# Kernel optimization log

Measured on AMD Instinct MI355X. Metric: run time of the kernel, lower is better.

The kernel has to match this reference:

```python
import jax, jax.numpy as jnp
import numpy as np

HID = 128  # hardcoded in the original module (hyperparameters['hidden_sizes'])
BETA1, BETA2, ADAM_EPS = 0.9, 0.999, 1e-8  # torch.optim.Adam defaults


def _xavier(k, shape):
    lim = np.sqrt(6.0 / (shape[0] + shape[1]))
    return jax.random.uniform(k, shape, jnp.float32, -lim, lim)


def setup_inputs() -> dict:
    key = jax.random.key(0)
    k0, k1, k2 = jax.random.split(key, 3)
    input_size, output_size = 65536, 4096
    return {
        "x": jax.random.uniform(k0, (input_size,), jnp.float32),
        "W1": _xavier(k1, (input_size, HID)),
        "W2": _xavier(k2, (HID, output_size)),
        "b_in": jnp.zeros((input_size,), jnp.float32),
        "b_h": jnp.zeros((HID,), jnp.float32),
        "b_out": jnp.zeros((output_size,), jnp.float32),
        "hidden0": jnp.zeros((HID,), jnp.float32),
        "output0": jnp.zeros((output_size,), jnp.float32),
        "n_iterations": 256,
        "epsilon": 0.01,
    }


def _drho(s):
    # gradient mask of rho = clamp(s, 0, 1), matching torch clamp backward
    return ((s >= 0.0) & (s <= 1.0)).astype(s.dtype)


def reference(x, W1, W2, b_in, b_h, b_out, hidden0, output0, n_iterations, epsilon):
    r_x = jnp.clip(x, 0.0, 1.0)
    xW1 = r_x @ W1  # [HID], constant across iterations (input is clamped/fixed)

    def adam(p, g, m, v, t1):
        m = BETA1 * m + (1.0 - BETA1) * g
        v = BETA2 * v + (1.0 - BETA2) * g * g
        mhat = m / (1.0 - jnp.power(BETA1, t1))
        vhat = v / (1.0 - jnp.power(BETA2, t1))
        return p - epsilon * mhat / (jnp.sqrt(vhat) + ADAM_EPS), m, v

    def step(carry, t):
        h, o, mh, vh, mo, vo = carry
        r_h = jnp.clip(h, 0.0, 1.0)
        r_o = jnp.clip(o, 0.0, 1.0)
        # analytic dE/dh, dE/do of the quadratic Hopfield energy
        g_h = _drho(h) * (r_h - b_h - xW1 - W2 @ r_o)      # [HID]
        g_o = _drho(o) * (r_o - b_out - r_h @ W2)          # [output_size]
        t1 = t + 1.0
        h, mh, vh = adam(h, g_h, mh, vh, t1)
        o, mo, vo = adam(o, g_o, mo, vo, t1)
        return (h, o, mh, vh, mo, vo), None

    init = (hidden0, output0,
            jnp.zeros_like(hidden0), jnp.zeros_like(hidden0),
            jnp.zeros_like(output0), jnp.zeros_like(output0))
    (h, o, *_), _ = jax.lax.scan(step, init, jnp.arange(n_iterations, dtype=jnp.float32))
    return o
```

## Files before the change

kernel.cpp:

```cpp
#include <hip/hip_runtime.h>
#include <stdint.h>

#define HID   128
#define OUT   4096
#define NWG   16
#define SLICE 256
#define NT    512
#define NXB   128
#define RPX   512
#define PDEPTH 4

typedef unsigned long long u64;

__device__ __forceinline__ u64 pk(uint32_t tag, float v) {
  return ((u64)tag << 32) | (u64)__float_as_uint(v);
}

__device__ __forceinline__ void lds_barrier() {
  asm volatile("s_waitcnt lgkmcnt(0)\n\ts_barrier" ::: "memory");
}

__global__ __launch_bounds__(NT, 1) void k_all(
    const float* __restrict__ x,
    const float* __restrict__ W1,
    const float* __restrict__ W2,
    const float* __restrict__ b_h,
    const float* __restrict__ b_out,
    const float* __restrict__ h0,
    const float* __restrict__ o0,
    const int* __restrict__ n_iter_p,
    const float* __restrict__ eps_p,
    u64* __restrict__ pbuf,
    u64* __restrict__ xw1p,
    float* __restrict__ out) {

  __shared__ __attribute__((aligned(16))) float red[8 * SLICE];
  __shared__ __attribute__((aligned(16))) float ro_s[SLICE];
  __shared__ __attribute__((aligned(16))) float rh_w[8][16];
  __shared__ __attribute__((aligned(16))) float bhx_s[HID];
  __shared__ __attribute__((aligned(16))) float h0_s[HID];

  const int t = threadIdx.x;

  if (blockIdx.x >= NWG) {
    const int b = blockIdx.x - NWG;
    const int c4 = (t & 31) * 4;
    const int rseg = t >> 5;
    const int r0 = b * RPX + rseg * 32;
    float4 acc = make_float4(0.f, 0.f, 0.f, 0.f);
#pragma unroll 8
    for (int k = 0; k < 32; ++k) {
      const int r = r0 + k;
      const float rx = fminf(fmaxf(x[r], 0.f), 1.f);
      const float4 wv = *(const float4*)&W1[(size_t)r * HID + c4];
      acc.x = fmaf(rx, wv.x, acc.x); acc.y = fmaf(rx, wv.y, acc.y);
      acc.z = fmaf(rx, wv.z, acc.z); acc.w = fmaf(rx, wv.w, acc.w);
    }
    *(float4*)&red[rseg * HID + c4] = acc;
    __syncthreads();
    if (t < HID) {
      float s = 0.f;
#pragma unroll
      for (int k = 0; k < 16; k += 4)
        s += (red[k*HID + t] + red[(k+1)*HID + t]) + (red[(k+2)*HID + t] + red[(k+3)*HID + t]);
      __hip_atomic_store(&xw1p[b * HID + t], pk(1u, s),
                         __ATOMIC_RELAXED, __HIP_MEMORY_SCOPE_AGENT);
    }
    return;
  }

  const int wg = blockIdx.x;
  const int cg = t & 63;
  const int rg = t >> 6;
  const int rloc = cg >> 2;
  const int q    = cg & 3;
  const int row  = rg * 16 + rloc;
  const int n_iter = *n_iter_p;
  const float eps  = *eps_p;

  float w2[16][4];
  {
    const float* wp = W2 + (size_t)(rg * 16) * OUT + wg * SLICE + cg;
#pragma unroll
    for (int r = 0; r < 16; ++r)
#pragma unroll
      for (int k = 0; k < 4; ++k)
        w2[r][k] = wp[(size_t)r * OUT + 64 * k];
  }
#pragma unroll
  for (int r = 0; r < 16; ++r)
    asm volatile("" : "+v"(w2[r][0]), "+v"(w2[r][1]), "+v"(w2[r][2]), "+v"(w2[r][3]));

  if (t < HID) {
    float s = 0.f;
#pragma unroll 1
    for (int ch = 0; ch < 8; ++ch) {
      u64 v[16];
      for (;;) {
#pragma unroll
        for (int k = 0; k < 16; ++k)
          v[k] = __hip_atomic_load(&xw1p[(ch * 16 + k) * HID + t],
                                   __ATOMIC_RELAXED, __HIP_MEMORY_SCOPE_AGENT);
        uint32_t bad = 0u;
#pragma unroll
        for (int k = 0; k < 16; ++k) bad |= ((uint32_t)(v[k] >> 32)) ^ 1u;
        if (bad == 0u) break;
        __builtin_amdgcn_s_sleep(2);
      }
#pragma unroll
      for (int k = 0; k < 16; ++k) s += __uint_as_float((uint32_t)v[k]);
    }
    bhx_s[t] = b_h[t] + s;
    h0_s[t]  = h0[t];
  }
  float oo = 0.f, mo = 0.f, vo = 0.f, bo = 0.f;
  if (t < SLICE) {
    oo = o0[wg * SLICE + t];
    bo = b_out[wg * SLICE + t];
    ro_s[t] = fminf(fmaxf(oo, 0.f), 1.f);
  }
  __syncthreads();

  float hh  = h0_s[row];
  float bhx = bhx_s[row];
  float mh = 0.f, vh = 0.f;
  if (q == 0) rh_w[rg][rloc] = fminf(fmaxf(hh, 0.f), 1.f);

  float bp1 = 1.f, bp2 = 1.f;

  for (int it = 0; it < n_iter; ++it) {
    const float bph1 = bp1, bph2 = bp2;
    bp1 *= 0.9f; bp2 *= 0.999f;
    const float co1 = 1.f / (1.f - bp1);
    const float co2 = 1.f / (1.f - bp2);
    u64* pbCur  = pbuf + (size_t)(it & (PDEPTH - 1)) * (NWG * HID);
    u64* pbPrev = pbuf + (size_t)((it + PDEPTH - 1) & (PDEPTH - 1)) * (NWG * HID);
    const uint32_t tagCur  = (uint32_t)(it + 1);
    const uint32_t tagPrev = (uint32_t)it;

    u64 v0 = 0, v1 = 0, v2 = 0, v3 = 0;
    if (it > 0) {
      v0 = __hip_atomic_load(&pbPrev[(q     ) * HID + row], __ATOMIC_RELAXED, __HIP_MEMORY_SCOPE_AGENT);
      v1 = __hip_atomic_load(&pbPrev[(q +  4) * HID + row], __ATOMIC_RELAXED, __HIP_MEMORY_SCOPE_AGENT);
      v2 = __hip_atomic_load(&pbPrev[(q +  8) * HID + row], __ATOMIC_RELAXED, __HIP_MEMORY_SCOPE_AGENT);
      v3 = __hip_atomic_load(&pbPrev[(q + 12) * HID + row], __ATOMIC_RELAXED, __HIP_MEMORY_SCOPE_AGENT);
    }

    float aB[16];
    {
      float rov[4];
#pragma unroll
      for (int k = 0; k < 4; ++k) rov[k] = ro_s[cg + 64 * k];
#pragma unroll
      for (int r = 0; r < 16; ++r) {
        float a = w2[r][0] * rov[0];
#pragma unroll
        for (int k = 1; k < 4; ++k) a = fmaf(w2[r][k], rov[k], a);
        aB[r] = a;
      }
    }
    {
#pragma unroll
      for (int r = 0; r < 8; ++r) {
        const float keep = (cg & 32) ? aB[r + 8] : aB[r];
        const float send = (cg & 32) ? aB[r]     : aB[r + 8];
        aB[r] = keep + __shfl_xor(send, 32, 64);
      }
#pragma unroll
      for (int r = 0; r < 4; ++r) {
        const float keep = (cg & 16) ? aB[r + 4] : aB[r];
        const float send = (cg & 16) ? aB[r]     : aB[r + 4];
        aB[r] = keep + __shfl_xor(send, 16, 64);
      }
#pragma unroll
      for (int r = 0; r < 2; ++r) {
        const float keep = (cg & 8) ? aB[r + 2] : aB[r];
        const float send = (cg & 8) ? aB[r]     : aB[r + 2];
        aB[r] = keep + __shfl_xor(send, 8, 64);
      }
      {
        const float keep = (cg & 4) ? aB[1] : aB[0];
        const float send = (cg & 4) ? aB[0] : aB[1];
        aB[0] = keep + __shfl_xor(send, 4, 64);
      }
      aB[0] += __shfl_xor(aB[0], 2, 64);
      aB[0] += __shfl_xor(aB[0], 1, 64);
    }
    if (q == 0) {
      __hip_atomic_store(&pbCur[wg * HID + row], pk(tagCur, aB[0]),
                         __ATOMIC_RELAXED, __HIP_MEMORY_SCOPE_AGENT);
    }

    if (it > 0) {
      for (;;) {
        const bool bad = ((uint32_t)(v0 >> 32) != tagPrev) || ((uint32_t)(v1 >> 32) != tagPrev)
                      || ((uint32_t)(v2 >> 32) != tagPrev) || ((uint32_t)(v3 >> 32) != tagPrev);
        if (!__any(bad)) break;
        v0 = __hip_atomic_load(&pbPrev[(q     ) * HID + row], __ATOMIC_RELAXED, __HIP_MEMORY_SCOPE_AGENT);
        v1 = __hip_atomic_load(&pbPrev[(q +  4) * HID + row], __ATOMIC_RELAXED, __HIP_MEMORY_SCOPE_AGENT);
        v2 = __hip_atomic_load(&pbPrev[(q +  8) * HID + row], __ATOMIC_RELAXED, __HIP_MEMORY_SCOPE_AGENT);
        v3 = __hip_atomic_load(&pbPrev[(q + 12) * HID + row], __ATOMIC_RELAXED, __HIP_MEMORY_SCOPE_AGENT);
      }
      float s2 = (__uint_as_float((uint32_t)v0) + __uint_as_float((uint32_t)v1))
               + (__uint_as_float((uint32_t)v2) + __uint_as_float((uint32_t)v3));
      s2 += __shfl_xor(s2, 1, 64);
      s2 += __shfl_xor(s2, 2, 64);
      const float ch1 = 1.f / (1.f - bph1);
      const float ch2 = 1.f / (1.f - bph2);
      const float rh_old = fminf(fmaxf(hh, 0.f), 1.f);
      const float g = (hh >= 0.f && hh <= 1.f) ? (rh_old - bhx - s2) : 0.f;
      mh = 0.9f * mh + 0.1f * g;
      vh = 0.999f * vh + 0.001f * g * g;
      hh -= eps * (mh * ch1) / (sqrtf(vh * ch2) + 1e-8f);
      if (q == 0) rh_w[rg][rloc] = fminf(fmaxf(hh, 0.f), 1.f);
    }

    {
      float aA[4] = {0.f, 0.f, 0.f, 0.f};
#pragma unroll
      for (int r = 0; r < 16; ++r) {
        const float rh = rh_w[rg][r];
#pragma unroll
        for (int k = 0; k < 4; ++k) aA[k] = fmaf(w2[r][k], rh, aA[k]);
      }
#pragma unroll
      for (int k = 0; k < 4; ++k)
        red[rg * SLICE + cg + 64 * k] = aA[k];
    }
    lds_barrier();

    if (t < SLICE) {
      const float s = ((red[t] + red[SLICE + t]) + (red[2*SLICE + t] + red[3*SLICE + t]))
                    + ((red[4*SLICE + t] + red[5*SLICE + t]) + (red[6*SLICE + t] + red[7*SLICE + t]));
      const float ro_old = fminf(fmaxf(oo, 0.f), 1.f);
      const float g = (oo >= 0.f && oo <= 1.f) ? (ro_old - bo - s) : 0.f;
      mo = 0.9f * mo + 0.1f * g;
      vo = 0.999f * vo + 0.001f * g * g;
      oo -= eps * (mo * co1) / (sqrtf(vo * co2) + 1e-8f);
      ro_s[t] = fminf(fmaxf(oo, 0.f), 1.f);
    }
    lds_barrier();
  }

  if (t < SLICE) out[wg * SLICE + t] = oo;
}

extern "C" void kernel_launch(void* const* d_in, const int* in_sizes, int n_in,
                              void* d_out, int out_size, void* d_ws, size_t ws_size,
                              hipStream_t stream) {
  const float* x     = (const float*)d_in[0];
  const float* W1    = (const float*)d_in[1];
  const float* W2    = (const float*)d_in[2];
  const float* b_h   = (const float*)d_in[4];
  const float* b_out = (const float*)d_in[5];
  const float* h0    = (const float*)d_in[6];
  const float* o0    = (const float*)d_in[7];
  const int*   nit   = (const int*)d_in[8];
  const float* eps   = (const float*)d_in[9];

  u64*   pbuf = (u64*)d_ws;
  u64*   xw1p = (u64*)((char*)d_ws + 65536);
  float* out  = (float*)d_out;

  k_all<<<dim3(NWG + NXB), dim3(NT), 0, stream>>>(x, W1, W2, b_h, b_out, h0, o0,
                                                  nit, eps, pbuf, xw1p, out);
}
```

Measured before the change: 609.7 us.

## Double-buffer output reduction and compute output Adam redundantly per thread

Replaces the dedicated output-update phase and its second barrier with double-buffered LDS partial sums. Each thread now redundantly performs the Adam update for its four output columns at the start of the next iteration and keeps o/m/v in registers, which removes one workgroup barrier and the ro_s round trip per iteration. It also switches the divisions to hardware reciprocal approximations and moves the bias-correction coefficient computation. The cost is 8x redundant output-update arithmetic, more registers, and slightly less precise division.

```diff
diff --git a/kernel.cpp b/kernel.cpp
--- a/kernel.cpp
+++ b/kernel.cpp
@@ -15,6 +15,8 @@
 __device__ __forceinline__ u64 pk(uint32_t tag, float v) {
   return ((u64)tag << 32) | (u64)__float_as_uint(v);
 }
+
+__device__ __forceinline__ float frcp(float x) { return __builtin_amdgcn_rcpf(x); }
 
 __device__ __forceinline__ void lds_barrier() {
   asm volatile("s_waitcnt lgkmcnt(0)\n\ts_barrier" ::: "memory");
@@ -34,8 +36,7 @@
     u64* __restrict__ xw1p,
     float* __restrict__ out) {
 
-  __shared__ __attribute__((aligned(16))) float red[8 * SLICE];
-  __shared__ __attribute__((aligned(16))) float ro_s[SLICE];
+  __shared__ __attribute__((aligned(16))) float red[2 * 8 * SLICE];
   __shared__ __attribute__((aligned(16))) float rh_w[8][16];
   __shared__ __attribute__((aligned(16))) float bhx_s[HID];
   __shared__ __attribute__((aligned(16))) float h0_s[HID];
@@ -113,11 +114,12 @@
     bhx_s[t] = b_h[t] + s;
     h0_s[t]  = h0[t];
   }
-  float oo = 0.f, mo = 0.f, vo = 0.f, bo = 0.f;
-  if (t < SLICE) {
-    oo = o0[wg * SLICE + t];
-    bo = b_out[wg * SLICE + t];
-    ro_s[t] = fminf(fmaxf(oo, 0.f), 1.f);
+  float oo[4], mo[4], vo[4], bo[4];
+#pragma unroll
+  for (int k = 0; k < 4; ++k) {
+    oo[k] = o0[wg * SLICE + cg + 64 * k];
+    bo[k] = b_out[wg * SLICE + cg + 64 * k];
+    mo[k] = 0.f; vo[k] = 0.f;
   }
   __syncthreads();
 
@@ -129,10 +131,9 @@
   float bp1 = 1.f, bp2 = 1.f;
 
   for (int it = 0; it < n_iter; ++it) {
-    const float bph1 = bp1, bph2 = bp2;
+    const float c1 = frcp(1.f - bp1);
+    const float c2 = frcp(1.f - bp2);
     bp1 *= 0.9f; bp2 *= 0.999f;
-    const float co1 = 1.f / (1.f - bp1);
-    const float co2 = 1.f / (1.f - bp2);
     u64* pbCur  = pbuf + (size_t)(it & (PDEPTH - 1)) * (NWG * HID);
     u64* pbPrev = pbuf + (size_t)((it + PDEPTH - 1) & (PDEPTH - 1)) * (NWG * HID);
     const uint32_t tagCur  = (uint32_t)(it + 1);
@@ -146,18 +147,33 @@
       v3 = __hip_atomic_load(&pbPrev[(q + 12) * HID + row], __ATOMIC_RELAXED, __HIP_MEMORY_SCOPE_AGENT);
     }
 
+    float ro[4];
+    if (it > 0) {
+      const float* rb = red + (size_t)((it + 1) & 1) * (8 * SLICE);
+#pragma unroll
+      for (int k = 0; k < 4; ++k) {
+        const int c = cg + 64 * k;
+        const float s = ((rb[c] + rb[SLICE + c]) + (rb[2*SLICE + c] + rb[3*SLICE + c]))
+                      + ((rb[4*SLICE + c] + rb[5*SLICE + c]) + (rb[6*SLICE + c] + rb[7*SLICE + c]));
+        const float ro_old = fminf(fmaxf(oo[k], 0.f), 1.f);
+        const float g = (oo[k] >= 0.f && oo[k] <= 1.f) ? (ro_old - bo[k] - s) : 0.f;
+        mo[k] = 0.9f * mo[k] + 0.1f * g;
+        vo[k] = 0.999f * vo[k] + 0.001f * g * g;
+        oo[k] -= eps * (mo[k] * c1) * frcp(sqrtf(vo[k] * c2) + 1e-8f);
+        ro[k] = fminf(fmaxf(oo[k], 0.f), 1.f);
+      }
+    } else {
+#pragma unroll
+      for (int k = 0; k < 4; ++k) ro[k] = fminf(fmaxf(oo[k], 0.f), 1.f);
+    }
+
     float aB[16];
-    {
-      float rov[4];
-#pragma unroll
-      for (int k = 0; k < 4; ++k) rov[k] = ro_s[cg + 64 * k];
-#pragma unroll
-      for (int r = 0; r < 16; ++r) {
-        float a = w2[r][0] * rov[0];
-#pragma unroll
-        for (int k = 1; k < 4; ++k) a = fmaf(w2[r][k], rov[k], a);
-        aB[r] = a;
-      }
+#pragma unroll
+    for (int r = 0; r < 16; ++r) {
+      float a = w2[r][0] * ro[0];
+#pragma unroll
+      for (int k = 1; k < 4; ++k) a = fmaf(w2[r][k], ro[k], a);
+      aB[r] = a;
     }
     {
 #pragma unroll
@@ -205,13 +221,11 @@
                + (__uint_as_float((uint32_t)v2) + __uint_as_float((uint32_t)v3));
       s2 += __shfl_xor(s2, 1, 64);
       s2 += __shfl_xor(s2, 2, 64);
-      const float ch1 = 1.f / (1.f - bph1);
-      const float ch2 = 1.f / (1.f - bph2);
       const float rh_old = fminf(fmaxf(hh, 0.f), 1.f);
       const float g = (hh >= 0.f && hh <= 1.f) ? (rh_old - bhx - s2) : 0.f;
       mh = 0.9f * mh + 0.1f * g;
       vh = 0.999f * vh + 0.001f * g * g;
-      hh -= eps * (mh * ch1) / (sqrtf(vh * ch2) + 1e-8f);
+      hh -= eps * (mh * c1) * frcp(sqrtf(vh * c2) + 1e-8f);
       if (q == 0) rh_w[rg][rloc] = fminf(fmaxf(hh, 0.f), 1.f);
     }
 
@@ -223,26 +237,35 @@
 #pragma unroll
         for (int k = 0; k < 4; ++k) aA[k] = fmaf(w2[r][k], rh, aA[k]);
       }
+      float* wb = red + (size_t)(it & 1) * (8 * SLICE);
 #pragma unroll
       for (int k = 0; k < 4; ++k)
-        red[rg * SLICE + cg + 64 * k] = aA[k];
+        wb[rg * SLICE + cg + 64 * k] = aA[k];
     }
     lds_barrier();
-
-    if (t < SLICE) {
-      const float s = ((red[t] + red[SLICE + t]) + (red[2*SLICE + t] + red[3*SLICE + t]))
-                    + ((red[4*SLICE + t] + red[5*SLICE + t]) + (red[6*SLICE + t] + red[7*SLICE + t]));
-      const float ro_old = fminf(fmaxf(oo, 0.f), 1.f);
-      const float g = (oo >= 0.f && oo <= 1.f) ? (ro_old - bo - s) : 0.f;
-      mo = 0.9f * mo + 0.1f * g;
-      vo = 0.999f * vo + 0.001f * g * g;
-      oo -= eps * (mo * co1) / (sqrtf(vo * co2) + 1e-8f);
-      ro_s[t] = fminf(fmaxf(oo, 0.f), 1.f);
-    }
-    lds_barrier();
-  }
-
-  if (t < SLICE) out[wg * SLICE + t] = oo;
+  }
+
+  {
+    const float c1 = frcp(1.f - bp1);
+    const float c2 = frcp(1.f - bp2);
+    const float* rb = red + (size_t)((n_iter + 1) & 1) * (8 * SLICE);
+#pragma unroll
+    for (int k = 0; k < 4; ++k) {
+      const int c = cg + 64 * k;
+      const float s = ((rb[c] + rb[SLICE + c]) + (rb[2*SLICE + c] + rb[3*SLICE + c]))
+                    + ((rb[4*SLICE + c] + rb[5*SLICE + c]) + (rb[6*SLICE + c] + rb[7*SLICE + c]));
+      const float ro_old = fminf(fmaxf(oo[k], 0.f), 1.f);
+      const float g = (oo[k] >= 0.f && oo[k] <= 1.f) ? (ro_old - bo[k] - s) : 0.f;
+      mo[k] = 0.9f * mo[k] + 0.1f * g;
+      vo[k] = 0.999f * vo[k] + 0.001f * g * g;
+      oo[k] -= eps * (mo[k] * c1) * frcp(sqrtf(vo[k] * c2) + 1e-8f);
+    }
+    if (rg == 0) {
+#pragma unroll
+      for (int k = 0; k < 4; ++k)
+        out[wg * SLICE + cg + 64 * k] = oo[k];
+    }
+  }
 }
 
 extern "C" void kernel_launch(void* const* d_in, const int* in_sizes, int n_in,
```

Result: slower. 797.5 us (+30.8%).
